# Kernel optimization log

Hardware: AMD Instinct MI355X
Metric: run time of the kernel (lower is better)

Reference implementation:

```python
import math
import jax, jax.numpy as jnp
import numpy as np
from jax.scipy.linalg import solve_triangular

K, D, Q = 512, 2048, 8
B = 8192
EPS = 1e-5
RHO0 = math.log(math.exp(1.0) - 1.0)  # softplus^-1(1.0), matches psi_init=scale_init=1.0


def setup_inputs() -> dict:
    key = jax.random.key(0)
    k1, k2, k3, k4, k5 = jax.random.split(key, 5)
    x = jax.random.normal(k1, (B, D), dtype=jnp.float32)
    mu = jax.random.normal(k2, (K, D), dtype=jnp.float32)          # centroids
    dir_raw = jax.random.normal(k3, (K, D, Q), dtype=jnp.float32) / math.sqrt(D)
    scale_rho = jnp.full((K, Q), RHO0, dtype=jnp.float32) + 0.01 * jax.random.normal(k4, (K, Q), dtype=jnp.float32)
    psi_rho = jnp.full((D,), RHO0, dtype=jnp.float32) + 0.01 * jax.random.normal(k5, (D,), dtype=jnp.float32)
    pi_logits = jnp.zeros((K,), dtype=jnp.float32)
    return {"x": x, "mu": mu, "dir_raw": dir_raw, "scale_rho": scale_rho,
            "psi_rho": psi_rho, "pi_logits": pi_logits}


def _nll(x, mu, dir_raw, scale_rho, psi_rho, pi_logits):
    Dd = x.shape[1]
    q = dir_raw.shape[2]
    # diagonal noise (shared across components since psi_per_component=False)
    psi = jax.nn.softplus(psi_rho) + EPS                      # (D,)
    psi_inv = 1.0 / psi                                       # (D,)
    # factor loadings W_k = normalize(dir_raw, dim=1) * softplus(scale)
    n = jnp.maximum(jnp.linalg.norm(dir_raw, axis=1, keepdims=True), EPS)
    W = (dir_raw / n) * jax.nn.softplus(scale_rho)[:, None, :]  # (K, D, q)
    # Woodbury inner matrix M_k = I + W^T Psi^{-1} W and its Cholesky
    A = W * jnp.sqrt(psi_inv)[None, :, None]                  # (K, D, q)
    M = jnp.einsum('kdi,kdj->kij', A, A) + jnp.eye(q, dtype=W.dtype)[None]
    L = jnp.linalg.cholesky(M)                                # (K, q, q) lower
    # quadratic form pieces
    xT_Pinv_x = (x ** 2) @ psi_inv                            # (B,)
    xT_Pinv_mu = x @ (psi_inv[None, :] * mu).T                # (B, K)
    muT_Pinv_mu = jnp.sum(mu ** 2 * psi_inv[None, :], axis=-1)  # (K,)
    quad_Psi = xT_Pinv_x[:, None] - 2.0 * xT_Pinv_mu + muT_Pinv_mu[None, :]
    PinvW = psi_inv[None, :, None] * W                        # (K, D, q)
    WT_Pinv_x = jnp.einsum('bd,kdq->bkq', x, PinvW)           # (B, K, q)
    WT_Pinv_mu = jnp.einsum('kd,kdq->kq', mu, PinvW)          # (K, q)
    v = WT_Pinv_x - WT_Pinv_mu[None, :, :]                    # (B, K, q)
    # Ez = M^{-1} v via the Cholesky factor (batched over K, rhs over B)
    vT = jnp.transpose(v, (1, 2, 0))                          # (K, q, B)
    y = solve_triangular(L, vT, lower=True)
    EzT = solve_triangular(jnp.swapaxes(L, -1, -2), y, lower=False)
    Ez = jnp.transpose(EzT, (2, 0, 1))                        # (B, K, q)
    quad = quad_Psi - jnp.sum(v * Ez, axis=-1)                # (B, K)
    # log-determinants via Woodbury: log|C| = log|Psi| + log|M|
    logdet_Psi = jnp.sum(jnp.log(psi))                        # scalar (shared psi)
    logdet_M = 2.0 * jnp.sum(jnp.log(jnp.diagonal(L, axis1=-2, axis2=-1)), axis=-1)  # (K,)
    logdet_C = logdet_Psi + logdet_M                          # (K,)
    ll = -0.5 * (Dd * math.log(2.0 * math.pi) + logdet_C[None, :] + quad)  # (B, K)
    log_pi = jax.nn.log_softmax(pi_logits)
    logp = jax.scipy.special.logsumexp(ll + log_pi[None, :], axis=1)  # (B,)
    return jnp.mean(-logp)


def reference(x, mu, dir_raw, scale_rho, psi_rho, pi_logits):
    return _nll(x, mu, dir_raw, scale_rho, psi_rho, pi_logits)
```

## Files before the change

### kernel.cpp

```cpp
#include <hip/hip_runtime.h>

constexpr int Bn = 8192;
constexpr int Dd = 2048;
constexpr int Kk = 512;
constexpr int Qq = 8;
constexpr int Nn = Kk * 9;
constexpr float DLOG2PI = 3763.9722f;

constexpr int BM = 256, BN = 288, BK = 128;
constexpr int NT = Dd / BK;

constexpr float SX = 16.f;
constexpr float SW = 64.f;
constexpr float SG = 16.f;
constexpr float INV_UW = 1.f / (16.f * 64.f);
constexpr float INV_UG = 1.f / (16.f * 16.f);

constexpr size_t OFF_PSI   = 0;
constexpr size_t OFF_LDP   = 8192;
constexpr size_t OFF_LOGPI = 8448;
constexpr size_t OFF_OFFK  = 10752;
constexpr size_t OFF_MINV  = 13056;
constexpr size_t OFF_XPX   = 144384;
constexpr size_t OFF_XBF   = 177408;
constexpr size_t OFF_GT    = 33731840;
constexpr size_t OFF_LL    = 52606208;
constexpr size_t OFF_PART  = 69383424;

constexpr int LDS_AS   = 0;
constexpr int LDS_BS   = 65536;
constexpr int LDS_MINV = 139264;
constexpr int LDS_OFFC = 147584;
constexpr int LDS_TOT  = 147712;

typedef float f32x4 __attribute__((ext_vector_type(4)));
typedef int   i32x4v __attribute__((ext_vector_type(4)));
typedef int   i32x8v __attribute__((ext_vector_type(8)));

__device__ inline float softplusf(float x) {
  return fmaxf(x, 0.f) + log1pf(expf(-fabsf(x)));
}
__device__ inline unsigned short f2bf(float x) {
  unsigned int u = __builtin_bit_cast(unsigned int, x);
  u = (u + 0x7fffu + ((u >> 16) & 1u)) >> 16;
  return (unsigned short)u;
}
__device__ inline unsigned int pack2(float a, float b) {
  return (unsigned int)f2bf(a) | ((unsigned int)f2bf(b) << 16);
}
__device__ inline float bf2f(unsigned int u16) {
  unsigned int v = u16 << 16;
  return __builtin_bit_cast(float, v);
}
__device__ inline unsigned char f2fp8(float x) {
  int v = __builtin_amdgcn_cvt_pk_fp8_f32(x, 0.f, 0, false);
  return (unsigned char)(v & 0xff);
}
__device__ inline void glds16(const unsigned char* g, char* l) {
  __builtin_amdgcn_global_load_lds(
      (const __attribute__((address_space(1))) unsigned int*)g,
      (__attribute__((address_space(3))) unsigned int*)l, 16, 0, 0);
}
__device__ inline i32x8v ld_frag(const char* rowp, int quad, int s8) {
  i32x4v lo = *(const i32x4v*)(rowp + (((2 * quad)     ^ s8) * 16));
  i32x4v hi = *(const i32x4v*)(rowp + (((2 * quad + 1) ^ s8) * 16));
  i32x8v r;
  r[0] = lo[0]; r[1] = lo[1]; r[2] = lo[2]; r[3] = lo[3];
  r[4] = hi[0]; r[5] = hi[1]; r[6] = hi[2]; r[7] = hi[3];
  return r;
}

#define BARRIER()                                   \
  do {                                              \
    asm volatile("" ::: "memory");                  \
    __builtin_amdgcn_s_barrier();                   \
    asm volatile("" ::: "memory");                  \
  } while (0)

__global__ __launch_bounds__(256) void prep_psi(
    const float* __restrict__ psi_rho, const float* __restrict__ pi_logits,
    float* __restrict__ psi_inv, float* __restrict__ logdetPsi,
    float* __restrict__ logpi) {
  __shared__ float red[256];
  int t = threadIdx.x;
  float acc = 0.f;
  for (int d = t; d < Dd; d += 256) {
    float p = softplusf(psi_rho[d]) + 1e-5f;
    psi_inv[d] = 1.f / p;
    acc += logf(p);
  }
  red[t] = acc;
  __syncthreads();
  for (int s = 128; s > 0; s >>= 1) { if (t < s) red[t] += red[t + s]; __syncthreads(); }
  if (t == 0) *logdetPsi = red[0];
  __syncthreads();
  float mx = -3.4e38f;
  for (int i = t; i < Kk; i += 256) mx = fmaxf(mx, pi_logits[i]);
  red[t] = mx;
  __syncthreads();
  for (int s = 128; s > 0; s >>= 1) { if (t < s) red[t] = fmaxf(red[t], red[t + s]); __syncthreads(); }
  mx = red[0];
  __syncthreads();
  float se = 0.f;
  for (int i = t; i < Kk; i += 256) se += expf(pi_logits[i] - mx);
  red[t] = se;
  __syncthreads();
  for (int s = 128; s > 0; s >>= 1) { if (t < s) red[t] += red[t + s]; __syncthreads(); }
  float lse = mx + logf(red[0]);
  for (int i = t; i < Kk; i += 256) logpi[i] = pi_logits[i] - lse;
}

__global__ __launch_bounds__(256) void prep_all(
    const float* __restrict__ x, const float* __restrict__ mu,
    const float* __restrict__ dir_raw, const float* __restrict__ scale_rho,
    const float* __restrict__ psi_inv,
    float* __restrict__ offk, float* __restrict__ Minv,
    unsigned char* __restrict__ Gq, unsigned char* __restrict__ xq,
    float* __restrict__ xPx) {
  __shared__ unsigned short sDir[Dd * 8];
  __shared__ float sPwmd[Dd];
  __shared__ float redk[4 * 53];
  __shared__ float R[53];
  __shared__ float sAl[8], sAh[8];

  int bid = blockIdx.x;
  int t = threadIdx.x, lane = t & 63, w = t >> 6;

  if (bid >= Kk) {
    int b = bid - Kk;
    const float4* xr = (const float4*)(x + (size_t)b * Dd);
    const float4* pr = (const float4*)psi_inv;
    float4 v0 = xr[2 * t], v1 = xr[2 * t + 1];
    float4 p0 = pr[2 * t], p1 = pr[2 * t + 1];
    float acc = v0.x * v0.x * p0.x + v0.y * v0.y * p0.y + v0.z * v0.z * p0.z + v0.w * v0.w * p0.w
              + v1.x * v1.x * p1.x + v1.y * v1.y * p1.y + v1.z * v1.z * p1.z + v1.w * v1.w * p1.w;
    unsigned int q0 = (unsigned int)__builtin_amdgcn_cvt_pk_fp8_f32(SX * v0.x, SX * v0.y, 0, false);
    q0 = (unsigned int)__builtin_amdgcn_cvt_pk_fp8_f32(SX * v0.z, SX * v0.w, (int)q0, true);
    unsigned int q1 = (unsigned int)__builtin_amdgcn_cvt_pk_fp8_f32(SX * v1.x, SX * v1.y, 0, false);
    q1 = (unsigned int)__builtin_amdgcn_cvt_pk_fp8_f32(SX * v1.z, SX * v1.w, (int)q1, true);
    uint2 o; o.x = q0; o.y = q1;
    *(uint2*)(xq + (size_t)b * Dd + t * 8) = o;
#pragma unroll
    for (int s2 = 32; s2; s2 >>= 1) acc += __shfl_down(acc, s2, 64);
    float* r4 = sPwmd;
    if (lane == 0) r4[w] = acc;
    __syncthreads();
    if (t == 0) xPx[b] = r4[0] + r4[1] + r4[2] + r4[3];
    return;
  }

  int k = bid;
  float vals[53];
#pragma unroll
  for (int i = 0; i < 53; i++) vals[i] = 0.f;
  const float4* dirp = (const float4*)(dir_raw + (size_t)k * Dd * Qq);
  for (int d = t; d < Dd; d += 256) {
    float4 da = dirp[d * 2], db = dirp[d * 2 + 1];
    float dir8[8] = {da.x, da.y, da.z, da.w, db.x, db.y, db.z, db.w};
    float pw = psi_inv[d];
    float md = mu[(size_t)k * Dd + d];
    int c = 0;
#pragma unroll
    for (int i = 0; i < 8; i++) {
      float dip = dir8[i] * pw;
#pragma unroll
      for (int j = 0; j < 8; j++) {
        if (j < i) continue;
        vals[c] += dip * dir8[j]; c++;
      }
    }
#pragma unroll
    for (int q = 0; q < 8; q++) vals[36 + q] += dir8[q] * dir8[q];
    float mp = md * pw;
#pragma unroll
    for (int q = 0; q < 8; q++) vals[44 + q] += mp * dir8[q];
    vals[52] += md * mp;
    uint4 pk;
    pk.x = pack2(pw * dir8[0], pw * dir8[1]);
    pk.y = pack2(pw * dir8[2], pw * dir8[3]);
    pk.z = pack2(pw * dir8[4], pw * dir8[5]);
    pk.w = pack2(pw * dir8[6], pw * dir8[7]);
    *(uint4*)(sDir + d * 8) = pk;
    sPwmd[d] = mp;
  }
#pragma unroll
  for (int v = 0; v < 53; v++) {
    float val = vals[v];
#pragma unroll
    for (int o = 32; o; o >>= 1) val += __shfl_down(val, o, 64);
    if (lane == 0) redk[w * 53 + v] = val;
  }
  __syncthreads();
  if (t < 53) R[t] = redk[t] + redk[53 + t] + redk[106 + t] + redk[159 + t];
  __syncthreads();
  if (t == 0) {
    float Sf[8][8];
    {
      int c2 = 0;
#pragma unroll
      for (int i = 0; i < 8; i++) {
#pragma unroll
        for (int j = 0; j < 8; j++) {
          if (j < i) continue;
          float v = R[c2++]; Sf[i][j] = v; Sf[j][i] = v;
        }
      }
    }
    float alpha[8];
#pragma unroll
    for (int q = 0; q < 8; q++) {
      float nr = fmaxf(sqrtf(R[36 + q]), 1e-5f);
      alpha[q] = softplusf(scale_rho[(size_t)k * 8 + q]) / nr;
    }
    float Mm[8][8];
#pragma unroll
    for (int i = 0; i < 8; i++)
#pragma unroll
      for (int j = 0; j < 8; j++)
        Mm[i][j] = alpha[i] * alpha[j] * Sf[i][j] + (i == j ? 1.f : 0.f);
    float L[8][8], Ld[8];
#pragma unroll
    for (int i = 0; i < 8; i++) {
#pragma unroll
      for (int j = 0; j < 8; j++) {
        if (j > i) continue;
        float s2 = Mm[i][j];
#pragma unroll
        for (int p = 0; p < 8; p++) { if (p < j) s2 -= L[i][p] * L[j][p]; }
        if (i == j) { L[i][i] = sqrtf(s2); Ld[i] = 1.f / L[i][i]; }
        else        L[i][j] = s2 * Ld[j];
      }
    }
    float logdetM = 0.f;
#pragma unroll
    for (int i = 0; i < 8; i++) logdetM += 2.f * logf(L[i][i]);
    float wv[8];
#pragma unroll
    for (int q = 0; q < 8; q++) wv[q] = alpha[q] * R[44 + q];
    float y[8], h[8];
#pragma unroll
    for (int i = 0; i < 8; i++) {
      float s2 = wv[i];
#pragma unroll
      for (int p = 0; p < 8; p++) { if (p < i) s2 -= L[i][p] * y[p]; }
      y[i] = s2 * Ld[i];
    }
#pragma unroll
    for (int i = 7; i >= 0; i--) {
      float s2 = y[i];
#pragma unroll
      for (int p = 0; p < 8; p++) { if (p > i) s2 -= L[p][i] * h[p]; }
      h[i] = s2 * Ld[i];
    }
    float cc = R[52];
#pragma unroll
    for (int q = 0; q < 8; q++) cc -= wv[q] * h[q];
#pragma unroll
    for (int col = 0; col < 8; col++) {
      float yy[8], z[8];
#pragma unroll
      for (int i = 0; i < 8; i++) {
        float s2 = (i == col) ? 1.f : 0.f;
#pragma unroll
        for (int p = 0; p < 8; p++) { if (p < i) s2 -= L[i][p] * yy[p]; }
        yy[i] = s2 * Ld[i];
      }
#pragma unroll
      for (int i = 7; i >= 0; i--) {
        float s2 = yy[i];
#pragma unroll
        for (int p = 0; p < 8; p++) { if (p > i) s2 -= L[p][i] * z[p]; }
        z[i] = s2 * Ld[i];
      }
#pragma unroll
      for (int r2 = 0; r2 < 8; r2++) Minv[(size_t)k * 64 + r2 * 8 + col] = z[r2];
    }
    offk[k] = -0.5f * (DLOG2PI + logdetM + cc);
#pragma unroll
    for (int q = 0; q < 8; q++) { sAl[q] = alpha[q]; sAh[q] = alpha[q] * h[q]; }
  }
  __syncthreads();
  float al[8], ah[8];
#pragma unroll
  for (int q = 0; q < 8; q++) { al[q] = sAl[q]; ah[q] = sAh[q]; }
  for (int d = t; d < Dd; d += 256) {
    uint4 pk = *(const uint4*)(sDir + d * 8);
    float pd[8];
    pd[0] = bf2f(pk.x & 0xffffu); pd[1] = bf2f(pk.x >> 16);
    pd[2] = bf2f(pk.y & 0xffffu); pd[3] = bf2f(pk.y >> 16);
    pd[4] = bf2f(pk.z & 0xffffu); pd[5] = bf2f(pk.z >> 16);
    pd[6] = bf2f(pk.w & 0xffffu); pd[7] = bf2f(pk.w >> 16);
    float gs = 0.f;
#pragma unroll
    for (int q = 0; q < 8; q++) {
      Gq[((size_t)(k * 9 + q)) * Dd + d] = f2fp8(SW * al[q] * pd[q]);
      gs += ah[q] * pd[q];
    }
    Gq[((size_t)(k * 9 + 8)) * Dd + d] = f2fp8(SG * (sPwmd[d] - gs));
  }
}

#define MFMA_COL(nt, bv)                                              \
  do {                                                                \
    acc[0][nt] = __builtin_amdgcn_mfma_scale_f32_16x16x128_f8f6f4(    \
        a0, bv, acc[0][nt], 0, 0, 0, 0x7f7f7f7f, 0, 0x7f7f7f7f);      \
    acc[1][nt] = __builtin_amdgcn_mfma_scale_f32_16x16x128_f8f6f4(    \
        a1, bv, acc[1][nt], 0, 0, 0, 0x7f7f7f7f, 0, 0x7f7f7f7f);      \
    acc[2][nt] = __builtin_amdgcn_mfma_scale_f32_16x16x128_f8f6f4(    \
        a2, bv, acc[2][nt], 0, 0, 0, 0x7f7f7f7f, 0, 0x7f7f7f7f);      \
    acc[3][nt] = __builtin_amdgcn_mfma_scale_f32_16x16x128_f8f6f4(    \
        a3, bv, acc[3][nt], 0, 0, 0, 0x7f7f7f7f, 0, 0x7f7f7f7f);      \
  } while (0)

__global__ __launch_bounds__(512, 1) void gemm_ll(
    const unsigned char* __restrict__ xq, const unsigned char* __restrict__ Gq,
    const float* __restrict__ Minv, const float* __restrict__ offk,
    const float* __restrict__ logpi, const float* __restrict__ logdetPsi,
    const float* __restrict__ xPx, float* __restrict__ ll) {
  __shared__ __align__(16) char smem[LDS_TOT];
  float* Cs    = (float*)smem;
  float* sMinv = (float*)(smem + LDS_MINV);
  float* sOff  = (float*)(smem + LDS_OFFC);

  int t = threadIdx.x, lane = t & 63, w = t >> 6;
  int wr = w >> 1, wc = w & 1;
  int m0 = blockIdx.y * BM;
  int n0 = blockIdx.x * BN;
  int comp0 = blockIdx.x * 32;

  for (int i = t; i < 2048; i += 512) {
    int cl = i >> 6, idx = i & 63;
    sMinv[cl * 65 + idx] = Minv[(size_t)comp0 * 64 + i];
  }
  if (t < 32)
    sOff[t] = offk[comp0 + t] + logpi[comp0 + t] - 0.5f * logdetPsi[0];

  f32x4 acc[4][9];
  f32x4 zero = {0.f, 0.f, 0.f, 0.f};
#pragma unroll
  for (int mt = 0; mt < 4; mt++)
#pragma unroll
    for (int nt = 0; nt < 9; nt++) acc[mt][nt] = zero;

  int rr  = lane >> 3;
  int cph = lane & 7;
  int csw = cph ^ rr;
  int quad = lane >> 4, r16 = lane & 15;
  int s8 = r16 & 7;
  const int aoff = (wr * 64 + r16) * 128;
  const int boff = (wc * 144 + r16) * 128;

  auto stage = [&](int buf, int k0) {
    if (w < 4) {
      char* dst = smem + LDS_AS + buf * 32768 + w * 8192;
      const unsigned char* src =
          xq + (size_t)(m0 + w * 64 + rr) * Dd + k0 + csw * 16;
#pragma unroll
      for (int i = 0; i < 8; ++i)
        glds16(src + (size_t)i * 8 * Dd, dst + i * 1024);
    } else {
      int w4 = w - 4;
      char* dst = smem + LDS_BS + buf * 36864 + w4 * 9216;
      const unsigned char* src =
          Gq + (size_t)(n0 + w4 * 72 + rr) * Dd + k0 + csw * 16;
#pragma unroll
      for (int i = 0; i < 9; ++i)
        glds16(src + (size_t)i * 8 * Dd, dst + i * 1024);
    }
  };

  stage(0, 0);
  asm volatile("s_waitcnt vmcnt(0) lgkmcnt(0)" ::: "memory");
  BARRIER();

#pragma unroll 1
  for (int tt = 0; tt < NT; ++tt) {
    int cur = tt & 1;
    const char* Ab = smem + LDS_AS + cur * 32768;
    const char* Bb = smem + LDS_BS + cur * 36864;
    if (tt < NT - 1) stage(cur ^ 1, (tt + 1) * BK);
    i32x8v a0 = ld_frag(Ab + aoff,        quad, s8);
    i32x8v a1 = ld_frag(Ab + aoff + 2048, quad, s8);
    i32x8v a2 = ld_frag(Ab + aoff + 4096, quad, s8);
    i32x8v a3 = ld_frag(Ab + aoff + 6144, quad, s8);
#pragma unroll
    for (int nt = 0; nt < 9; ++nt) {
      i32x8v bv = ld_frag(Bb + boff + nt * 2048, quad, s8);
      MFMA_COL(nt, bv);
    }
    asm volatile("s_waitcnt vmcnt(0)" ::: "memory");
    BARRIER();
  }

  float P[36];
  {
    const float* Mi = sMinv + (wc * 16 + r16) * 65;
    int c = 0;
#pragma unroll
    for (int i2 = 0; i2 < 8; i2++) {
      P[c++] = 0.5f * Mi[i2 * 8 + i2];
#pragma unroll
      for (int j2 = i2 + 1; j2 < 8; j2++) P[c++] = Mi[i2 * 8 + j2];
    }
  }
  float offc = sOff[wc * 16 + r16];

  float* myC = Cs + w * (16 * 148);
#pragma unroll
  for (int mt = 0; mt < 4; ++mt) {
#pragma unroll
    for (int nt = 0; nt < 9; ++nt) {
#pragma unroll
      for (int r = 0; r < 4; r++) {
        myC[(quad * 4 + r) * 148 + nt * 16 + r16] = acc[mt][nt][r];
      }
    }
#pragma unroll
    for (int i = 0; i < 4; i++) {
      int row_l = quad + 4 * i;
      int b = m0 + wr * 64 + mt * 16 + row_l;
      const float* cp = myC + row_l * 148 + r16 * 9;
      float u[8];
#pragma unroll
      for (int j = 0; j < 8; j++) u[j] = cp[j] * INV_UW;
      float s = cp[8] * INV_UG;
      float tq = 0.f;
      int c = 0;
#pragma unroll
      for (int i2 = 0; i2 < 8; i2++) {
        float s2 = P[c++] * u[i2];
#pragma unroll
        for (int j2 = i2 + 1; j2 < 8; j2++) s2 += P[c++] * u[j2];
        tq += u[i2] * s2;
      }
      ll[(size_t)b * Kk + comp0 + wc * 16 + r16] = offc + s + tq - 0.5f * xPx[b];
    }
  }
}

__global__ __launch_bounds__(256) void lse_rows(
    const float* __restrict__ ll, float* __restrict__ part) {
  int t = threadIdx.x, lane = t & 63, w = t >> 6;
  int b = blockIdx.x * 4 + w;
  const float* row = ll + (size_t)b * Kk;
  float v[8];
  float mx = -3.4e38f;
#pragma unroll
  for (int i = 0; i < 8; i++) { v[i] = row[lane + 64 * i]; mx = fmaxf(mx, v[i]); }
#pragma unroll
  for (int o = 32; o; o >>= 1) mx = fmaxf(mx, __shfl_xor(mx, o, 64));
  float se = 0.f;
#pragma unroll
  for (int i = 0; i < 8; i++) se += expf(v[i] - mx);
#pragma unroll
  for (int o = 32; o; o >>= 1) se += __shfl_xor(se, o, 64);
  __shared__ float r4[4];
  if (lane == 0) r4[w] = -(mx + logf(se));
  __syncthreads();
  if (t == 0) part[blockIdx.x] = r4[0] + r4[1] + r4[2] + r4[3];
}

__global__ __launch_bounds__(256) void final_mean(
    const float* __restrict__ part, float* __restrict__ out) {
  int t = threadIdx.x, lane = t & 63, w = t >> 6;
  float acc = 0.f;
  for (int i = t; i < 2048; i += 256) acc += part[i];
#pragma unroll
  for (int o = 32; o; o >>= 1) acc += __shfl_down(acc, o, 64);
  __shared__ float r4[4];
  if (lane == 0) r4[w] = acc;
  __syncthreads();
  if (t == 0) out[0] = (r4[0] + r4[1] + r4[2] + r4[3]) * (1.0f / 8192.0f);
}

extern "C" void kernel_launch(void* const* d_in, const int* in_sizes, int n_in,
                              void* d_out, int out_size, void* d_ws, size_t ws_size,
                              hipStream_t stream) {
  const float* x         = (const float*)d_in[0];
  const float* mu        = (const float*)d_in[1];
  const float* dir_raw   = (const float*)d_in[2];
  const float* scale_rho = (const float*)d_in[3];
  const float* psi_rho   = (const float*)d_in[4];
  const float* pi_logits = (const float*)d_in[5];
  float* out = (float*)d_out;
  char* ws = (char*)d_ws;

  float* psi_inv          = (float*)(ws + OFF_PSI);
  float* logdetPsi        = (float*)(ws + OFF_LDP);
  float* logpi            = (float*)(ws + OFF_LOGPI);
  float* offk             = (float*)(ws + OFF_OFFK);
  float* Minv             = (float*)(ws + OFF_MINV);
  float* xPx              = (float*)(ws + OFF_XPX);
  unsigned char* xq       = (unsigned char*)(ws + OFF_XBF);
  unsigned char* Gq       = (unsigned char*)(ws + OFF_GT);
  float* ll               = (float*)(ws + OFF_LL);
  float* part             = (float*)(ws + OFF_PART);

  prep_psi<<<1, 256, 0, stream>>>(psi_rho, pi_logits, psi_inv, logdetPsi, logpi);
  prep_all<<<Kk + Bn, 256, 0, stream>>>(x, mu, dir_raw, scale_rho, psi_inv,
                                        offk, Minv, Gq, xq, xPx);
  dim3 g(Nn / BN, Bn / BM);
  gemm_ll<<<g, 512, 0, stream>>>(xq, Gq, Minv, offk, logpi, logdetPsi, xPx, ll);
  lse_rows<<<Bn / 4, 256, 0, stream>>>(ll, part);
  final_mean<<<1, 256, 0, stream>>>(part, out);
}
```

Baseline: 226.7 us.

## Software-pipeline B fragment loads with MFMAs and parallelize Minv column solves

The GEMM inner loop now double-buffers B-fragment LDS reads so that each column's fragment is loaded while the previous column's MFMAs run, with sched_group_barrier hints telling the compiler how to interleave DS reads and MFMAs. In the prep kernel, the 8 triangular solves that form M^-1, previously run serially by one thread, are spread across 8 threads using the Cholesky factor staged in shared memory. The aim is to hide LDS latency behind matrix math and to shorten the serial tail of the prep kernel, at the cost of extra registers and a rigid hand-written schedule.

```diff
diff --git a/kernel.cpp b/kernel.cpp
--- a/kernel.cpp
+++ b/kernel.cpp
@@ -76,6 +76,8 @@
     __builtin_amdgcn_s_barrier();                   \
     asm volatile("" ::: "memory");                  \
   } while (0)
+
+#define SGB(mask, n) __builtin_amdgcn_sched_group_barrier((mask), (n), 0)
 
 __global__ __launch_bounds__(256) void prep_psi(
     const float* __restrict__ psi_rho, const float* __restrict__ pi_logits,
@@ -109,6 +111,8 @@
   float lse = mx + logf(red[0]);
   for (int i = t; i < Kk; i += 256) logpi[i] = pi_logits[i] - lse;
 }
+
+#define TRI(i, j) ((i) * ((i) + 1) / 2 + (j))
 
 __global__ __launch_bounds__(256) void prep_all(
     const float* __restrict__ x, const float* __restrict__ mu,
@@ -122,6 +126,7 @@
   __shared__ float redk[4 * 53];
   __shared__ float R[53];
   __shared__ float sAl[8], sAh[8];
+  __shared__ float sLt[36], sLdt[8];
 
   int bid = blockIdx.x;
   int t = threadIdx.x, lane = t & 63, w = t >> 6;
@@ -255,31 +260,40 @@
     float cc = R[52];
 #pragma unroll
     for (int q = 0; q < 8; q++) cc -= wv[q] * h[q];
-#pragma unroll
-    for (int col = 0; col < 8; col++) {
-      float yy[8], z[8];
-#pragma unroll
-      for (int i = 0; i < 8; i++) {
-        float s2 = (i == col) ? 1.f : 0.f;
-#pragma unroll
-        for (int p = 0; p < 8; p++) { if (p < i) s2 -= L[i][p] * yy[p]; }
-        yy[i] = s2 * Ld[i];
-      }
-#pragma unroll
-      for (int i = 7; i >= 0; i--) {
-        float s2 = yy[i];
-#pragma unroll
-        for (int p = 0; p < 8; p++) { if (p > i) s2 -= L[p][i] * z[p]; }
-        z[i] = s2 * Ld[i];
-      }
-#pragma unroll
-      for (int r2 = 0; r2 < 8; r2++) Minv[(size_t)k * 64 + r2 * 8 + col] = z[r2];
+    {
+      int c3 = 0;
+#pragma unroll
+      for (int i = 0; i < 8; i++)
+#pragma unroll
+        for (int j = 0; j < 8; j++) { if (j <= i) sLt[c3++] = L[i][j]; }
+#pragma unroll
+      for (int i = 0; i < 8; i++) sLdt[i] = Ld[i];
     }
     offk[k] = -0.5f * (DLOG2PI + logdetM + cc);
 #pragma unroll
     for (int q = 0; q < 8; q++) { sAl[q] = alpha[q]; sAh[q] = alpha[q] * h[q]; }
   }
   __syncthreads();
+  if (t < 8) {
+    int col = t;
+    float yy[8], z[8];
+#pragma unroll
+    for (int i = 0; i < 8; i++) {
+      float s2 = (i == col) ? 1.f : 0.f;
+#pragma unroll
+      for (int p = 0; p < 8; p++) { if (p < i) s2 -= sLt[TRI(i, p)] * yy[p]; }
+      yy[i] = s2 * sLdt[i];
+    }
+#pragma unroll
+    for (int i = 7; i >= 0; i--) {
+      float s2 = yy[i];
+#pragma unroll
+      for (int p = 0; p < 8; p++) { if (p > i) s2 -= sLt[TRI(p, i)] * z[p]; }
+      z[i] = s2 * sLdt[i];
+    }
+#pragma unroll
+    for (int r2 = 0; r2 < 8; r2++) Minv[(size_t)k * 64 + r2 * 8 + col] = z[r2];
+  }
   float al[8], ah[8];
 #pragma unroll
   for (int q = 0; q < 8; q++) { al[q] = sAl[q]; ah[q] = sAh[q]; }
@@ -312,6 +326,12 @@
         a3, bv, acc[3][nt], 0, 0, 0, 0x7f7f7f7f, 0, 0x7f7f7f7f);      \
   } while (0)
 
+#define GSTEP(nt, CUR, NXT)                                           \
+  NXT = ld_frag(Bb + boff + ((nt) + 1) * 2048, quad, s8);             \
+  SGB(0x100, 2);                                                      \
+  MFMA_COL(nt, CUR);                                                  \
+  SGB(0x008, 4);
+
 __global__ __launch_bounds__(512, 1) void gemm_ll(
     const unsigned char* __restrict__ xq, const unsigned char* __restrict__ Gq,
     const float* __restrict__ Minv, const float* __restrict__ offk,
@@ -383,11 +403,19 @@
     i32x8v a1 = ld_frag(Ab + aoff + 2048, quad, s8);
     i32x8v a2 = ld_frag(Ab + aoff + 4096, quad, s8);
     i32x8v a3 = ld_frag(Ab + aoff + 6144, quad, s8);
-#pragma unroll
-    for (int nt = 0; nt < 9; ++nt) {
-      i32x8v bv = ld_frag(Bb + boff + nt * 2048, quad, s8);
-      MFMA_COL(nt, bv);
-    }
+    i32x8v bvX = ld_frag(Bb + boff, quad, s8);
+    i32x8v bvY;
+    SGB(0x100, 10);
+    GSTEP(0, bvX, bvY)
+    GSTEP(1, bvY, bvX)
+    GSTEP(2, bvX, bvY)
+    GSTEP(3, bvY, bvX)
+    GSTEP(4, bvX, bvY)
+    GSTEP(5, bvY, bvX)
+    GSTEP(6, bvX, bvY)
+    GSTEP(7, bvY, bvX)
+    MFMA_COL(8, bvX);
+    SGB(0x008, 4);
     asm volatile("s_waitcnt vmcnt(0)" ::: "memory");
     BARRIER();
   }
```

After: 224.1 us. About the same (-1.1%).

## Load A fragments directly from global memory and spread Minv solve over threads

Applied to the files above, without the earlier changes.

The GEMM kernel no longer stages the x (A) tile through LDS. Each wave loads its A fragments straight from global memory into registers, while all 8 waves share the work of staging the B (Gq) tile into LDS. This frees LDS and removes the A-side LDS reads, but the global A loads sit in the critical path with no double buffering, and each A row is fetched by two waves. Separately, the 8-column Minv triangular solve in prep_all is moved from one thread to 8 threads through shared-memory copies of L.

```diff
diff --git a/kernel.cpp b/kernel.cpp
--- a/kernel.cpp
+++ b/kernel.cpp
@@ -27,11 +27,11 @@
 constexpr size_t OFF_LL    = 52606208;
 constexpr size_t OFF_PART  = 69383424;
 
-constexpr int LDS_AS   = 0;
-constexpr int LDS_BS   = 65536;
-constexpr int LDS_MINV = 139264;
-constexpr int LDS_OFFC = 147584;
-constexpr int LDS_TOT  = 147712;
+constexpr int LDS_BS   = 0;
+constexpr int LDS_MINV = 73728;
+constexpr int LDS_OFFC = 82048;
+constexpr int LDS_CS   = 82176;
+constexpr int LDS_TOT  = 157952;
 
 typedef float f32x4 __attribute__((ext_vector_type(4)));
 typedef int   i32x4v __attribute__((ext_vector_type(4)));
@@ -64,6 +64,14 @@
 __device__ inline i32x8v ld_frag(const char* rowp, int quad, int s8) {
   i32x4v lo = *(const i32x4v*)(rowp + (((2 * quad)     ^ s8) * 16));
   i32x4v hi = *(const i32x4v*)(rowp + (((2 * quad + 1) ^ s8) * 16));
+  i32x8v r;
+  r[0] = lo[0]; r[1] = lo[1]; r[2] = lo[2]; r[3] = lo[3];
+  r[4] = hi[0]; r[5] = hi[1]; r[6] = hi[2]; r[7] = hi[3];
+  return r;
+}
+__device__ inline i32x8v ld_ga(const char* p) {
+  i32x4v lo = *(const i32x4v*)(p);
+  i32x4v hi = *(const i32x4v*)(p + 16);
   i32x8v r;
   r[0] = lo[0]; r[1] = lo[1]; r[2] = lo[2]; r[3] = lo[3];
   r[4] = hi[0]; r[5] = hi[1]; r[6] = hi[2]; r[7] = hi[3];
@@ -109,6 +117,8 @@
   float lse = mx + logf(red[0]);
   for (int i = t; i < Kk; i += 256) logpi[i] = pi_logits[i] - lse;
 }
+
+#define TRI(i, j) ((i) * ((i) + 1) / 2 + (j))
 
 __global__ __launch_bounds__(256) void prep_all(
     const float* __restrict__ x, const float* __restrict__ mu,
@@ -122,6 +132,7 @@
   __shared__ float redk[4 * 53];
   __shared__ float R[53];
   __shared__ float sAl[8], sAh[8];
+  __shared__ float sLt[36], sLdt[8];
 
   int bid = blockIdx.x;
   int t = threadIdx.x, lane = t & 63, w = t >> 6;
@@ -255,31 +266,40 @@
     float cc = R[52];
 #pragma unroll
     for (int q = 0; q < 8; q++) cc -= wv[q] * h[q];
-#pragma unroll
-    for (int col = 0; col < 8; col++) {
-      float yy[8], z[8];
-#pragma unroll
-      for (int i = 0; i < 8; i++) {
-        float s2 = (i == col) ? 1.f : 0.f;
-#pragma unroll
-        for (int p = 0; p < 8; p++) { if (p < i) s2 -= L[i][p] * yy[p]; }
-        yy[i] = s2 * Ld[i];
-      }
-#pragma unroll
-      for (int i = 7; i >= 0; i--) {
-        float s2 = yy[i];
-#pragma unroll
-        for (int p = 0; p < 8; p++) { if (p > i) s2 -= L[p][i] * z[p]; }
-        z[i] = s2 * Ld[i];
-      }
-#pragma unroll
-      for (int r2 = 0; r2 < 8; r2++) Minv[(size_t)k * 64 + r2 * 8 + col] = z[r2];
+    {
+      int c3 = 0;
+#pragma unroll
+      for (int i = 0; i < 8; i++)
+#pragma unroll
+        for (int j = 0; j < 8; j++) { if (j <= i) sLt[c3++] = L[i][j]; }
+#pragma unroll
+      for (int i = 0; i < 8; i++) sLdt[i] = Ld[i];
     }
     offk[k] = -0.5f * (DLOG2PI + logdetM + cc);
 #pragma unroll
     for (int q = 0; q < 8; q++) { sAl[q] = alpha[q]; sAh[q] = alpha[q] * h[q]; }
   }
   __syncthreads();
+  if (t < 8) {
+    int col = t;
+    float yy[8], z[8];
+#pragma unroll
+    for (int i = 0; i < 8; i++) {
+      float s2 = (i == col) ? 1.f : 0.f;
+#pragma unroll
+      for (int p = 0; p < 8; p++) { if (p < i) s2 -= sLt[TRI(i, p)] * yy[p]; }
+      yy[i] = s2 * sLdt[i];
+    }
+#pragma unroll
+    for (int i = 7; i >= 0; i--) {
+      float s2 = yy[i];
+#pragma unroll
+      for (int p = 0; p < 8; p++) { if (p > i) s2 -= sLt[TRI(p, i)] * z[p]; }
+      z[i] = s2 * sLdt[i];
+    }
+#pragma unroll
+    for (int r2 = 0; r2 < 8; r2++) Minv[(size_t)k * 64 + r2 * 8 + col] = z[r2];
+  }
   float al[8], ah[8];
 #pragma unroll
   for (int q = 0; q < 8; q++) { al[q] = sAl[q]; ah[q] = sAh[q]; }
@@ -318,9 +338,9 @@
     const float* __restrict__ logpi, const float* __restrict__ logdetPsi,
     const float* __restrict__ xPx, float* __restrict__ ll) {
   __shared__ __align__(16) char smem[LDS_TOT];
-  float* Cs    = (float*)smem;
   float* sMinv = (float*)(smem + LDS_MINV);
   float* sOff  = (float*)(smem + LDS_OFFC);
+  float* Cs    = (float*)(smem + LDS_CS);
 
   int t = threadIdx.x, lane = t & 63, w = t >> 6;
   int wr = w >> 1, wc = w & 1;
@@ -347,25 +367,26 @@
   int csw = cph ^ rr;
   int quad = lane >> 4, r16 = lane & 15;
   int s8 = r16 & 7;
-  const int aoff = (wr * 64 + r16) * 128;
   const int boff = (wc * 144 + r16) * 128;
+  const char* abase =
+      (const char*)xq + (size_t)(m0 + wr * 64 + r16) * Dd + quad * 32;
 
   auto stage = [&](int buf, int k0) {
+    char* dst = smem + LDS_BS + buf * 36864;
     if (w < 4) {
-      char* dst = smem + LDS_AS + buf * 32768 + w * 8192;
-      const unsigned char* src =
-          xq + (size_t)(m0 + w * 64 + rr) * Dd + k0 + csw * 16;
-#pragma unroll
-      for (int i = 0; i < 8; ++i)
-        glds16(src + (size_t)i * 8 * Dd, dst + i * 1024);
+#pragma unroll
+      for (int i = 0; i < 4; ++i) {
+        int j = w * 4 + i;
+        glds16(Gq + (size_t)(n0 + j * 8 + rr) * Dd + k0 + csw * 16,
+               dst + j * 1024);
+      }
     } else {
-      int w4 = w - 4;
-      char* dst = smem + LDS_BS + buf * 36864 + w4 * 9216;
-      const unsigned char* src =
-          Gq + (size_t)(n0 + w4 * 72 + rr) * Dd + k0 + csw * 16;
-#pragma unroll
-      for (int i = 0; i < 9; ++i)
-        glds16(src + (size_t)i * 8 * Dd, dst + i * 1024);
+#pragma unroll
+      for (int i = 0; i < 5; ++i) {
+        int j = 16 + (w - 4) * 5 + i;
+        glds16(Gq + (size_t)(n0 + j * 8 + rr) * Dd + k0 + csw * 16,
+               dst + j * 1024);
+      }
     }
   };
 
@@ -376,13 +397,13 @@
 #pragma unroll 1
   for (int tt = 0; tt < NT; ++tt) {
     int cur = tt & 1;
-    const char* Ab = smem + LDS_AS + cur * 32768;
     const char* Bb = smem + LDS_BS + cur * 36864;
-    if (tt < NT - 1) stage(cur ^ 1, (tt + 1) * BK);
-    i32x8v a0 = ld_frag(Ab + aoff,        quad, s8);
-    i32x8v a1 = ld_frag(Ab + aoff + 2048, quad, s8);
-    i32x8v a2 = ld_frag(Ab + aoff + 4096, quad, s8);
-    i32x8v a3 = ld_frag(Ab + aoff + 6144, quad, s8);
+    int k0 = tt * BK;
+    i32x8v a0 = ld_ga(abase + k0);
+    i32x8v a1 = ld_ga(abase + 32768 + k0);
+    i32x8v a2 = ld_ga(abase + 65536 + k0);
+    i32x8v a3 = ld_ga(abase + 98304 + k0);
+    if (tt < NT - 1) stage(cur ^ 1, k0 + BK);
 #pragma unroll
     for (int nt = 0; nt < 9; ++nt) {
       i32x8v bv = ld_frag(Bb + boff + nt * 2048, quad, s8);
```

Measured after the change: 265.8 us. +17.3%, slower.
